# Optimization experiments

Measured on AMD Instinct MI355X. Metric: run time of the kernel, lower is better.

Reference implementation:

```python
import jax, jax.numpy as jnp
import numpy as np

N_NODES = 50000
N_EDGES = 800000
D = 64
EPS = 1e-12  # torch F.normalize eps


def edge_softmax(e, dst, n):
    # softmax over incoming edges of each dst node, per feature channel
    m = jax.ops.segment_max(e, dst, num_segments=n)          # [N, D]
    ex = jnp.exp(e - m[dst])                                 # [E, D]
    s = jax.ops.segment_sum(ex, dst, num_segments=n)         # [N, D]
    return ex / s[dst]


def gat_layer(h, src, dst, W_src, b_src, W_dst, b_dst, n):
    # attention logits: u_mul_v
    e = h[src] * h[dst]                                      # [E, D]
    alpha = edge_softmax(e, dst, n)                          # [E, D]
    # transformed features (fc_dst computed in source but unused downstream)
    feat_src = jax.nn.relu(h @ W_src.T + b_src)              # [N, D]
    _feat_dst = jax.nn.relu(h @ W_dst.T + b_dst)             # [N, D] (dead, kept for fidelity)
    # message: u_mul_e, then scatter-sum to dst
    msg = feat_src[src] * alpha                              # [E, D]
    return jax.ops.segment_sum(msg, dst, num_segments=n)     # [N, D]


def l2_normalize(x):
    nrm = jnp.sqrt(jnp.sum(x * x, axis=1, keepdims=True))
    return x / jnp.maximum(nrm, EPS)


def setup_inputs() -> dict:
    key = jax.random.key(0)
    ks = jax.random.split(key, 10)
    scale = 1.0 / np.sqrt(D)
    return {
        "node_ids": jax.random.randint(ks[0], (N_NODES,), 0, N_NODES),
        "src": jax.random.randint(ks[1], (N_EDGES,), 0, N_NODES),
        "dst": jax.random.randint(ks[2], (N_EDGES,), 0, N_NODES),
        "embed_table": jax.random.normal(ks[3], (N_NODES, D), jnp.float32) * 0.1,
        "W_src_0": jax.random.normal(ks[4], (D, D), jnp.float32) * scale,
        "b_src_0": jnp.zeros((D,), jnp.float32),
        "W_dst_0": jax.random.normal(ks[5], (D, D), jnp.float32) * scale,
        "b_dst_0": jnp.zeros((D,), jnp.float32),
        "W_src_1": jax.random.normal(ks[6], (D, D), jnp.float32) * scale,
        "b_src_1": jnp.zeros((D,), jnp.float32),
        "W_dst_1": jax.random.normal(ks[7], (D, D), jnp.float32) * scale,
        "b_dst_1": jnp.zeros((D,), jnp.float32),
    }


def reference(node_ids, src, dst, embed_table,
              W_src_0, b_src_0, W_dst_0, b_dst_0,
              W_src_1, b_src_1, W_dst_1, b_dst_1):
    n = node_ids.shape[0]
    h0 = embed_table[node_ids]                               # [N, D]
    h1 = gat_layer(h0, src, dst, W_src_0, b_src_0, W_dst_0, b_dst_0, n)
    h2 = gat_layer(h1, src, dst, W_src_1, b_src_1, W_dst_1, b_dst_1, n)
    # cache = [h0, norm(h1), norm(h2)]; h passed forward unnormalized
    return jnp.concatenate([h0, l2_normalize(h1), l2_normalize(h2)], axis=1)  # [N, 3D]
```

## Files before the change

### kernel.cpp

```cpp
#include <hip/hip_runtime.h>
#include <math.h>

#define NN 50000
#define NE 800000
#define DD 64

typedef __attribute__((ext_vector_type(8))) short short8v;
typedef __attribute__((ext_vector_type(4))) float floatx4;

__device__ __forceinline__ unsigned bf16r(float x) {
  unsigned u = __float_as_uint(x);
  return (u + 0x7fffu + ((u >> 16) & 1u)) >> 16;
}


__global__ void k_zero(int4* __restrict__ p, int n4) {
  int i = blockIdx.x * 256 + threadIdx.x;
  if (i < n4) p[i] = make_int4(0, 0, 0, 0);
}

__global__ void k_hist(const int4* __restrict__ dst4, int* __restrict__ deg,
                       int4* __restrict__ pos4) {
  int q = blockIdx.x * 256 + threadIdx.x;
  if (q >= NE / 4) return;
  int4 dn = dst4[q];
  int4 p;
  p.x = atomicAdd(&deg[dn.x], 1);
  p.y = atomicAdd(&deg[dn.y], 1);
  p.z = atomicAdd(&deg[dn.z], 1);
  p.w = atomicAdd(&deg[dn.w], 1);
  pos4[q] = p;
}

__global__ void k_scan1(const int* __restrict__ deg, int* __restrict__ rp,
                        int* __restrict__ bsum) {
  __shared__ int tmp[1024];
  int t = threadIdx.x;
  int i = blockIdx.x * 1024 + t;
  int v = (i < NN) ? deg[i] : 0;
  tmp[t] = v;
  __syncthreads();
  for (int off = 1; off < 1024; off <<= 1) {
    int x = (t >= off) ? tmp[t - off] : 0;
    __syncthreads();
    tmp[t] += x;
    __syncthreads();
  }
  if (i < NN) rp[i] = tmp[t] - v;
  if (t == 1023) bsum[blockIdx.x] = tmp[1023];
}

__global__ void k_scan2(int* __restrict__ bsum, int nb) {
  int t = threadIdx.x;
  int orig = (t < nb) ? bsum[t] : 0;
  int v = orig;
#pragma unroll
  for (int off = 1; off < 64; off <<= 1) {
    int x = __shfl_up(v, off, 64);
    if (t >= off) v += x;
  }
  if (t < nb) bsum[t] = v - orig;
}

__global__ void k_scan3(int* __restrict__ rp, const int* __restrict__ bsum) {
  int i = blockIdx.x * 1024 + threadIdx.x;
  if (i < NN) rp[i] += bsum[blockIdx.x];
  if (i == 0) rp[NN] = NE;
}

__global__ void k_scatter(const int4* __restrict__ src4, const int4* __restrict__ dst4,
                          const int* __restrict__ rp, const int4* __restrict__ pos4,
                          int* __restrict__ ssrc) {
  int q = blockIdx.x * 256 + threadIdx.x;
  if (q >= NE / 4) return;
  int4 s = src4[q], dn = dst4[q], p = pos4[q];
  ssrc[rp[dn.x] + p.x] = s.x;
  ssrc[rp[dn.y] + p.y] = s.y;
  ssrc[rp[dn.z] + p.z] = s.z;
  ssrc[rp[dn.w] + p.w] = s.w;
}

__global__ void __launch_bounds__(256) k_fc_mfma(const float* __restrict__ h,
                                                 const int* __restrict__ ids,
                                                 const float* __restrict__ W,
                                                 const float* __restrict__ b,
                                                 unsigned* __restrict__ hfb) {
  int lane = threadIdx.x & 63;
  int wid = threadIdx.x >> 6;
  int nbase = blockIdx.x * 64 + wid * 16;
  if (nbase >= NN) return;
  int r16 = lane & 15, kg = lane >> 4;

  int rowA = ids ? ids[nbase + r16] : (nbase + r16);
  const float* hrow = h + (size_t)rowA * DD;
  short8v afr[2];
#pragma unroll
  for (int kt = 0; kt < 2; ++kt) {
    int k0 = kt * 32 + kg * 8;
#pragma unroll
    for (int i = 0; i < 8; ++i) afr[kt][i] = (short)bf16r(hrow[k0 + i]);
  }
  int orow[4];
#pragma unroll
  for (int r = 0; r < 4; ++r) {
    int node = nbase + kg * 4 + r;
    orow[r] = ids ? ids[node] : node;
  }
  short8v bfr[4][2];
#pragma unroll
  for (int dt = 0; dt < 4; ++dt) {
    const float* wrow = W + (dt * 16 + r16) * 64;
#pragma unroll
    for (int kt = 0; kt < 2; ++kt) {
      int k0 = kt * 32 + kg * 8;
#pragma unroll
      for (int i = 0; i < 8; ++i) bfr[dt][kt][i] = (short)bf16r(wrow[k0 + i]);
    }
  }
#pragma unroll
  for (int dt = 0; dt < 4; ++dt) {
    floatx4 acc = {0.f, 0.f, 0.f, 0.f};
    acc = __builtin_amdgcn_mfma_f32_16x16x32_bf16(afr[0], bfr[dt][0], acc, 0, 0, 0);
    acc = __builtin_amdgcn_mfma_f32_16x16x32_bf16(afr[1], bfr[dt][1], acc, 0, 0, 0);
    int d = dt * 16 + r16;
    float bias = b[d];
#pragma unroll
    for (int r = 0; r < 4; ++r) {
      int node = nbase + kg * 4 + r;
      float feat = fmaxf(acc[r] + bias, 0.f);
      float hv = h[(size_t)orow[r] * DD + d];
      hfb[node * DD + d] = bf16r(hv) | (bf16r(feat) << 16);
    }
  }
}

__global__ void __launch_bounds__(256) k_edge(const unsigned* __restrict__ hfb,
                                              const float* __restrict__ h,
                                              const int* __restrict__ ids,
                                              const int* __restrict__ rp,
                                              const int* __restrict__ ssrc,
                                              float* __restrict__ hout, int ostride) {
  int d = threadIdx.x & 63;
  int node = blockIdx.x * 4 + (threadIdx.x >> 6);
  if (node >= NN) return;
  int beg = rp[node], end = rp[node + 1];
  int hrow = ids ? ids[node] : node;
  float hd = h[(size_t)hrow * DD + d];
  float s[8] = {0.f, 0.f, 0.f, 0.f, 0.f, 0.f, 0.f, 0.f};
  float a[8] = {0.f, 0.f, 0.f, 0.f, 0.f, 0.f, 0.f, 0.f};
  int lim = end - 1;
  for (int p = beg; p < end; p += 8) {
    unsigned v[8];
#pragma unroll
    for (int j = 0; j < 8; ++j) {
      int q = p + j;
      q = (q > lim) ? lim : q;
      v[j] = hfb[ssrc[q] * DD + d];
    }
#pragma unroll
    for (int j = 0; j < 8; ++j) {
      float hv = __uint_as_float(v[j] << 16);
      float fv = __uint_as_float(v[j] & 0xffff0000u);
      float ex = (p + j < end) ? __expf(hv * hd) : 0.f;
      s[j] += ex;
      a[j] = fmaf(fv, ex, a[j]);
    }
  }
  float ss = ((s[0] + s[1]) + (s[2] + s[3])) + ((s[4] + s[5]) + (s[6] + s[7]));
  float aa = ((a[0] + a[1]) + (a[2] + a[3])) + ((a[4] + a[5]) + (a[6] + a[7]));
  hout[node * ostride + d] = (end > beg) ? aa / ss : 0.f;
}

__global__ void __launch_bounds__(256) k_final(const float* __restrict__ emb,
                                               const int* __restrict__ ids,
                                               const float* __restrict__ h1,
                                               float* __restrict__ out) {
  int d = threadIdx.x & 63;
  int node = blockIdx.x * 4 + (threadIdx.x >> 6);
  if (node >= NN) return;
  float v1 = h1[node * DD + d], v2 = out[node * 192 + 128 + d];
  float s1 = v1 * v1, s2 = v2 * v2;
#pragma unroll
  for (int off = 32; off > 0; off >>= 1) {
    s1 += __shfl_xor(s1, off, 64);
    s2 += __shfl_xor(s2, off, 64);
  }
  out[node * 192 + d] = emb[(size_t)ids[node] * DD + d];
  out[node * 192 + 64 + d] = v1 / fmaxf(sqrtf(s1), 1e-12f);
  out[node * 192 + 128 + d] = v2 / fmaxf(sqrtf(s2), 1e-12f);
}


extern "C" void kernel_launch(void* const* d_in, const int* in_sizes, int n_in,
                              void* d_out, int out_size, void* d_ws, size_t ws_size,
                              hipStream_t stream) {
  const int* node_ids = (const int*)d_in[0];
  const int* src = (const int*)d_in[1];
  const int* dst = (const int*)d_in[2];
  const float* emb = (const float*)d_in[3];
  const float* W0 = (const float*)d_in[4];
  const float* b0 = (const float*)d_in[5];
  const float* W1 = (const float*)d_in[8];
  const float* b1 = (const float*)d_in[9];
  float* out = (float*)d_out;

  size_t o = 0;
  auto alloc = [&](size_t nbytes) {
    char* p = (char*)d_ws + o;
    o += (nbytes + 255) & ~(size_t)255;
    return (void*)p;
  };
  float* h1 = (float*)alloc((size_t)NN * DD * 4);
  unsigned* hfb = (unsigned*)alloc((size_t)NN * DD * 4);
  int* deg = (int*)alloc((size_t)(NN + 12) * 4);
  int* rp = (int*)alloc((size_t)(NN + 1) * 4);
  int* bsum = (int*)alloc(64 * 4);
  int* ssrc = (int*)alloc((size_t)NE * 4);
  int* pos = (int*)alloc((size_t)NE * 4);
  (void)o; (void)ws_size; (void)in_sizes; (void)n_in; (void)out_size;

  int n4 = (NN + 3) / 4;
  k_zero<<<(n4 + 255) / 256, 256, 0, stream>>>((int4*)deg, n4);
  k_hist<<<(NE / 4 + 255) / 256, 256, 0, stream>>>((const int4*)dst, deg, (int4*)pos);
  int NB = (NN + 1023) / 1024;
  k_scan1<<<NB, 1024, 0, stream>>>(deg, rp, bsum);
  k_scan2<<<1, 64, 0, stream>>>(bsum, NB);
  k_scan3<<<NB, 1024, 0, stream>>>(rp, bsum);
  k_scatter<<<(NE / 4 + 255) / 256, 256, 0, stream>>>(
      (const int4*)src, (const int4*)dst, rp, (const int4*)pos, ssrc);

  k_fc_mfma<<<(NN + 63) / 64, 256, 0, stream>>>(emb, node_ids, W0, b0, hfb);
  k_edge<<<(NN + 3) / 4, 256, 0, stream>>>(hfb, emb, node_ids, rp, ssrc, h1, DD);
  k_fc_mfma<<<(NN + 63) / 64, 256, 0, stream>>>(h1, nullptr, W1, b1, hfb);
  k_edge<<<(NN + 3) / 4, 256, 0, stream>>>(hfb, h1, nullptr, rp, ssrc, out + 128, 192);

  k_final<<<(NN + 3) / 4, 256, 0, stream>>>(emb, node_ids, h1, out);
}
```

Measured before the change: 177.6 us.

## Fuse zeroing into FC, merge scan passes, fuse final normalize into edge kernel

```diff
diff --git a/kernel.cpp b/kernel.cpp
--- a/kernel.cpp
+++ b/kernel.cpp
@@ -4,6 +4,9 @@
 #define NN 50000
 #define NE 800000
 #define DD 64
+#define FC_BLOCKS 782
+#define N4 12500
+#define ZB 49
 
 typedef __attribute__((ext_vector_type(8))) short short8v;
 typedef __attribute__((ext_vector_type(4))) float floatx4;
@@ -13,11 +16,6 @@
   return (u + 0x7fffu + ((u >> 16) & 1u)) >> 16;
 }
 
-
-__global__ void k_zero(int4* __restrict__ p, int n4) {
-  int i = blockIdx.x * 256 + threadIdx.x;
-  if (i < n4) p[i] = make_int4(0, 0, 0, 0);
-}
 
 __global__ void k_hist(const int4* __restrict__ dst4, int* __restrict__ deg,
                        int4* __restrict__ pos4) {
@@ -34,37 +32,45 @@
 
 __global__ void k_scan1(const int* __restrict__ deg, int* __restrict__ rp,
                         int* __restrict__ bsum) {
-  __shared__ int tmp[1024];
+  __shared__ int woff[16];
   int t = threadIdx.x;
   int i = blockIdx.x * 1024 + t;
   int v = (i < NN) ? deg[i] : 0;
-  tmp[t] = v;
+  int lane = t & 63, w = t >> 6;
+  int sc = v;
+#pragma unroll
+  for (int off = 1; off < 64; off <<= 1) {
+    int x = __shfl_up(sc, off, 64);
+    if (lane >= off) sc += x;
+  }
+  if (lane == 63) woff[w] = sc;
   __syncthreads();
-  for (int off = 1; off < 1024; off <<= 1) {
-    int x = (t >= off) ? tmp[t - off] : 0;
-    __syncthreads();
-    tmp[t] += x;
-    __syncthreads();
-  }
-  if (i < NN) rp[i] = tmp[t] - v;
-  if (t == 1023) bsum[blockIdx.x] = tmp[1023];
-}
-
-__global__ void k_scan2(int* __restrict__ bsum, int nb) {
-  int t = threadIdx.x;
-  int orig = (t < nb) ? bsum[t] : 0;
-  int v = orig;
-#pragma unroll
-  for (int off = 1; off < 64; off <<= 1) {
-    int x = __shfl_up(v, off, 64);
-    if (t >= off) v += x;
-  }
-  if (t < nb) bsum[t] = v - orig;
+  if (t < 16) {
+    int ws = woff[t];
+    int s2 = ws;
+#pragma unroll
+    for (int off = 1; off < 16; off <<= 1) {
+      int x = __shfl_up(s2, off, 64);
+      if (t >= off) s2 += x;
+    }
+    woff[t] = s2 - ws;
+    if (t == 15) bsum[blockIdx.x] = s2;
+  }
+  __syncthreads();
+  if (i < NN) rp[i] = sc - v + woff[w];
 }
 
 __global__ void k_scan3(int* __restrict__ rp, const int* __restrict__ bsum) {
+  __shared__ int soff;
+  if (threadIdx.x < 64) {
+    int v = ((int)threadIdx.x < (int)blockIdx.x) ? bsum[threadIdx.x] : 0;
+#pragma unroll
+    for (int off = 32; off > 0; off >>= 1) v += __shfl_xor(v, off, 64);
+    if (threadIdx.x == 0) soff = v;
+  }
+  __syncthreads();
   int i = blockIdx.x * 1024 + threadIdx.x;
-  if (i < NN) rp[i] += bsum[blockIdx.x];
+  if (i < NN) rp[i] += soff;
   if (i == 0) rp[NN] = NE;
 }
 
@@ -84,7 +90,13 @@
                                                  const int* __restrict__ ids,
                                                  const float* __restrict__ W,
                                                  const float* __restrict__ b,
-                                                 unsigned* __restrict__ hfb) {
+                                                 unsigned* __restrict__ hfb,
+                                                 int4* __restrict__ zbuf, int n4) {
+  if (blockIdx.x >= FC_BLOCKS) {
+    int i = (blockIdx.x - FC_BLOCKS) * 256 + threadIdx.x;
+    if (i < n4) zbuf[i] = make_int4(0, 0, 0, 0);
+    return;
+  }
   int lane = threadIdx.x & 63;
   int wid = threadIdx.x >> 6;
   int nbase = blockIdx.x * 64 + wid * 16;
@@ -134,12 +146,13 @@
   }
 }
 
-__global__ void __launch_bounds__(256) k_edge(const unsigned* __restrict__ hfb,
-                                              const float* __restrict__ h,
-                                              const int* __restrict__ ids,
-                                              const int* __restrict__ rp,
-                                              const int* __restrict__ ssrc,
-                                              float* __restrict__ hout, int ostride) {
+template <bool FINAL>
+__global__ void __launch_bounds__(256)
+k_edge_t(const unsigned* __restrict__ hfb, const float* __restrict__ h,
+         const int* __restrict__ ids, const int* __restrict__ rp,
+         const int* __restrict__ ssrc, float* __restrict__ outp, int ostride,
+         const float* __restrict__ emb, const int* __restrict__ fids,
+         const float* __restrict__ h1) {
   int d = threadIdx.x & 63;
   int node = blockIdx.x * 4 + (threadIdx.x >> 6);
   if (node >= NN) return;
@@ -149,45 +162,40 @@
   float s[8] = {0.f, 0.f, 0.f, 0.f, 0.f, 0.f, 0.f, 0.f};
   float a[8] = {0.f, 0.f, 0.f, 0.f, 0.f, 0.f, 0.f, 0.f};
   int lim = end - 1;
-  for (int p = beg; p < end; p += 8) {
-    unsigned v[8];
-#pragma unroll
-    for (int j = 0; j < 8; ++j) {
+  for (int p = beg; p < end; p += 16) {
+    unsigned v[16];
+#pragma unroll
+    for (int j = 0; j < 16; ++j) {
       int q = p + j;
       q = (q > lim) ? lim : q;
       v[j] = hfb[ssrc[q] * DD + d];
     }
 #pragma unroll
-    for (int j = 0; j < 8; ++j) {
+    for (int j = 0; j < 16; ++j) {
       float hv = __uint_as_float(v[j] << 16);
       float fv = __uint_as_float(v[j] & 0xffff0000u);
       float ex = (p + j < end) ? __expf(hv * hd) : 0.f;
-      s[j] += ex;
-      a[j] = fmaf(fv, ex, a[j]);
+      s[j & 7] += ex;
+      a[j & 7] = fmaf(fv, ex, a[j & 7]);
     }
   }
   float ss = ((s[0] + s[1]) + (s[2] + s[3])) + ((s[4] + s[5]) + (s[6] + s[7]));
   float aa = ((a[0] + a[1]) + (a[2] + a[3])) + ((a[4] + a[5]) + (a[6] + a[7]));
-  hout[node * ostride + d] = (end > beg) ? aa / ss : 0.f;
-}
-
-__global__ void __launch_bounds__(256) k_final(const float* __restrict__ emb,
-                                               const int* __restrict__ ids,
-                                               const float* __restrict__ h1,
-                                               float* __restrict__ out) {
-  int d = threadIdx.x & 63;
-  int node = blockIdx.x * 4 + (threadIdx.x >> 6);
-  if (node >= NN) return;
-  float v1 = h1[node * DD + d], v2 = out[node * 192 + 128 + d];
-  float s1 = v1 * v1, s2 = v2 * v2;
-#pragma unroll
-  for (int off = 32; off > 0; off >>= 1) {
-    s1 += __shfl_xor(s1, off, 64);
-    s2 += __shfl_xor(s2, off, 64);
-  }
-  out[node * 192 + d] = emb[(size_t)ids[node] * DD + d];
-  out[node * 192 + 64 + d] = v1 / fmaxf(sqrtf(s1), 1e-12f);
-  out[node * 192 + 128 + d] = v2 / fmaxf(sqrtf(s2), 1e-12f);
+  float hval = (end > beg) ? aa / ss : 0.f;
+  if (!FINAL) {
+    outp[(size_t)node * ostride + d] = hval;
+  } else {
+    float v1 = h1[(size_t)node * DD + d];
+    float s1 = v1 * v1, s2 = hval * hval;
+#pragma unroll
+    for (int off = 32; off > 0; off >>= 1) {
+      s1 += __shfl_xor(s1, off, 64);
+      s2 += __shfl_xor(s2, off, 64);
+    }
+    outp[node * 192 + d] = emb[(size_t)fids[node] * DD + d];
+    outp[node * 192 + 64 + d] = v1 / fmaxf(sqrtf(s1), 1e-12f);
+    outp[node * 192 + 128 + d] = hval / fmaxf(sqrtf(s2), 1e-12f);
+  }
 }
 
 
@@ -219,20 +227,18 @@
   int* pos = (int*)alloc((size_t)NE * 4);
   (void)o; (void)ws_size; (void)in_sizes; (void)n_in; (void)out_size;
 
-  int n4 = (NN + 3) / 4;
-  k_zero<<<(n4 + 255) / 256, 256, 0, stream>>>((int4*)deg, n4);
+  k_fc_mfma<<<FC_BLOCKS + ZB, 256, 0, stream>>>(emb, node_ids, W0, b0, hfb,
+                                                (int4*)deg, N4);
   k_hist<<<(NE / 4 + 255) / 256, 256, 0, stream>>>((const int4*)dst, deg, (int4*)pos);
   int NB = (NN + 1023) / 1024;
   k_scan1<<<NB, 1024, 0, stream>>>(deg, rp, bsum);
-  k_scan2<<<1, 64, 0, stream>>>(bsum, NB);
   k_scan3<<<NB, 1024, 0, stream>>>(rp, bsum);
   k_scatter<<<(NE / 4 + 255) / 256, 256, 0, stream>>>(
       (const int4*)src, (const int4*)dst, rp, (const int4*)pos, ssrc);
 
-  k_fc_mfma<<<(NN + 63) / 64, 256, 0, stream>>>(emb, node_ids, W0, b0, hfb);
-  k_edge<<<(NN + 3) / 4, 256, 0, stream>>>(hfb, emb, node_ids, rp, ssrc, h1, DD);
-  k_fc_mfma<<<(NN + 63) / 64, 256, 0, stream>>>(h1, nullptr, W1, b1, hfb);
-  k_edge<<<(NN + 3) / 4, 256, 0, stream>>>(hfb, h1, nullptr, rp, ssrc, out + 128, 192);
-
-  k_final<<<(NN + 3) / 4, 256, 0, stream>>>(emb, node_ids, h1, out);
-}
+  k_edge_t<false><<<(NN + 3) / 4, 256, 0, stream>>>(
+      hfb, emb, node_ids, rp, ssrc, h1, DD, nullptr, nullptr, nullptr);
+  k_fc_mfma<<<FC_BLOCKS, 256, 0, stream>>>(h1, nullptr, W1, b1, hfb, nullptr, 0);
+  k_edge_t<true><<<(NN + 3) / 4, 256, 0, stream>>>(
+      hfb, h1, nullptr, rp, ssrc, out, 0, emb, node_ids, h1);
+}
```

Result: faster. 172.3 us (-3.0%).
